# Optimization experiments

Hardware: AMD Instinct MI355X
Metric: run time of the kernel (lower is better)

The kernel has to match this reference:

```python
import jax, jax.numpy as jnp
import numpy as np

NC, NU, K, C, P, O = 20, 16, 128, 2048, 5, 256

def setup_inputs() -> dict:
    key = jax.random.key(0)
    ks = jax.random.split(key, 6)
    s = 0.02  # keep activations well-scaled
    return {
        "topk_feats": jax.random.normal(ks[0], (NC, NU, K, C), jnp.float32),
        "prototypes": jax.random.normal(ks[1], (NC, P, C), jnp.float32),
        "w_inner1": jax.random.normal(ks[2], (O, C), jnp.float32) * s,
        "w_inner_trans": jax.random.normal(ks[3], (C, C), jnp.float32) * s,
        "w_inter1": jax.random.normal(ks[4], (O, C), jnp.float32) * s,
        "w_inter2": jax.random.normal(ks[5], (O, C), jnp.float32) * s,
    }

def reference(topk_feats, prototypes, w_inner1, w_inner_trans, w_inter1, w_inter2):
    scale = 1.0 / jnp.sqrt(jnp.asarray(O, topk_feats.dtype))
    # --- inner (per-group) self-attention, vmapped over (class, unlabel) ---
    # fe: [nc, nu, k, o]
    fe = jnp.einsum("nukc,oc->nuko", topk_feats, w_inner1)
    att = jax.nn.softmax(jnp.einsum("nuko,nulo->nukl", fe, fe) * scale, axis=-1)
    agg = jnp.einsum("nukl,nulc->nukc", att, topk_feats)  # atte @ feat
    feats = topk_feats + jax.nn.relu(jnp.einsum("nukc,dc->nukd", agg, w_inner_trans))
    # --- inter (prototype -> all feats) cross-attention per class ---
    fa = feats.reshape(NC, NU * K, C)  # cat over unlabel dim
    fae = jnp.einsum("nmc,oc->nmo", fa, w_inter1)
    pe = jnp.einsum("npc,oc->npo", prototypes, w_inter2)
    att2 = jax.nn.softmax(jnp.einsum("npo,nmo->npm", pe, fae) * scale, axis=-1)
    un_protos = jnp.einsum("npm,nmc->npc", att2, fa)  # [nc, p, c]
    return un_protos
```

## Files before the change

kernel.cpp:

```cpp
#include <hip/hip_runtime.h>

typedef __attribute__((ext_vector_type(4))) float f32x4;
typedef __attribute__((ext_vector_type(8))) short short8;

#define DEVI static __device__ __forceinline__

DEVI unsigned short f2bf(float f) {
  unsigned int u = __float_as_uint(f);
  u += 0x7FFFu + ((u >> 16) & 1u);
  return (unsigned short)(u >> 16);
}
DEVI float bf2f(unsigned short s) { return __uint_as_float(((unsigned int)s) << 16); }
DEVI unsigned int pack2(float lo, float hi) {
  return ((unsigned int)f2bf(hi) << 16) | (unsigned int)f2bf(lo);
}

#define GL2LDS(gp, lp)                                                        \
  __builtin_amdgcn_global_load_lds(                                           \
      (const __attribute__((address_space(1))) void*)(const void*)(gp),       \
      (__attribute__((address_space(3))) void*)(void*)(lp), 16, 0, 0)

__global__ __launch_bounds__(256) void k_cvt_bf16(const float* __restrict__ src,
                                                  unsigned short* __restrict__ dst, int n4) {
  int i = blockIdx.x * 256 + threadIdx.x;
  if (i < n4) {
    float4 v = ((const float4*)src)[i];
    uint2 o; o.x = pack2(v.x, v.y); o.y = pack2(v.z, v.w);
    ((uint2*)dst)[i] = o;
  }
}

template <bool RES>
__global__ __launch_bounds__(256) void k_gemm_bt(const unsigned short* __restrict__ A,
                                                 const unsigned short* __restrict__ B,
                                                 unsigned short* __restrict__ C,
                                                 const float* __restrict__ resid, int N) {
  constexpr int K = 2048;
  __shared__ unsigned short lA[2][128 * 64];
  __shared__ unsigned short lB[2][128 * 64];
  const int tid = threadIdx.x;
  const int lane = tid & 63;
  const int wave = tid >> 6;
  const int wr = wave >> 1, wc = wave & 1;
  const int nx = gridDim.x;
  const int lin = blockIdx.y * nx + blockIdx.x;
  const int cpx = (nx * gridDim.y) >> 3;
  const int swz = (lin & 7) * cpx + (lin >> 3);
  const long mBase = (long)(swz / nx) * 128;
  const long nBase = (long)(swz % nx) * 128;

  f32x4 acc[4][4] = {};

  auto stage = [&](int buf, int k0) {
#pragma unroll
    for (int it = 0; it < 4; it++) {
      int idx = it * 256 + tid;
      int row = idx >> 3, kc = idx & 7;
      int skc = kc ^ (row & 7);
      int lbase = (it * 256 + (tid & ~63)) * 8;
      GL2LDS(A + (mBase + row) * (long)K + k0 + skc * 8, &lA[buf][lbase]);
      GL2LDS(B + (nBase + row) * (long)K + k0 + skc * 8, &lB[buf][lbase]);
    }
  };

  stage(0, 0);
  for (int t = 0; t < 32; t++) {
    const int cur = t & 1;
    if (t < 31) {
      stage(cur ^ 1, (t + 1) * 64);
      asm volatile("s_waitcnt vmcnt(8)" ::: "memory");
    } else {
      asm volatile("s_waitcnt vmcnt(0)" ::: "memory");
    }
    __builtin_amdgcn_s_barrier();
    __builtin_amdgcn_sched_barrier(0);
    const unsigned short* bA = &lA[cur][0];
    const unsigned short* bB = &lB[cur][0];
#pragma unroll
    for (int kb = 0; kb < 2; kb++) {
      short8 af[4], bfr[4];
#pragma unroll
      for (int mt = 0; mt < 4; mt++) {
        int row = wr * 64 + mt * 16 + (lane & 15);
        int slot = (kb * 4 + (lane >> 4)) ^ (row & 7);
        af[mt] = *(const short8*)&bA[row * 64 + slot * 8];
      }
#pragma unroll
      for (int nt = 0; nt < 4; nt++) {
        int row = wc * 64 + nt * 16 + (lane & 15);
        int slot = (kb * 4 + (lane >> 4)) ^ (row & 7);
        bfr[nt] = *(const short8*)&bB[row * 64 + slot * 8];
      }
#pragma unroll
      for (int mt = 0; mt < 4; mt++)
#pragma unroll
        for (int nt = 0; nt < 4; nt++)
          acc[mt][nt] = __builtin_amdgcn_mfma_f32_16x16x32_bf16(af[mt], bfr[nt], acc[mt][nt], 0, 0, 0);
    }
    __builtin_amdgcn_sched_barrier(0);
    __builtin_amdgcn_s_barrier();
  }
#pragma unroll
  for (int mt = 0; mt < 4; mt++) {
#pragma unroll
    for (int nt = 0; nt < 4; nt++) {
#pragma unroll
      for (int j = 0; j < 4; j++) {
        long row = mBase + wr * 64 + mt * 16 + (lane >> 4) * 4 + j;
        long col = nBase + wc * 64 + nt * 16 + (lane & 15);
        float v = acc[mt][nt][j];
        if constexpr (RES) v = resid[row * (long)N + col] + fmaxf(v, 0.0f);
        C[row * (long)N + col] = f2bf(v);
      }
    }
  }
}

template <bool RES>
__global__ __launch_bounds__(512, 2) void k_gemm256(const unsigned short* __restrict__ A,
                                                    const unsigned short* __restrict__ B,
                                                    unsigned short* __restrict__ C,
                                                    const float* __restrict__ resid, int N) {
  constexpr int K = 2048;
  __shared__ unsigned short lA[2][256 * 64];
  __shared__ unsigned short lB[2][256 * 64];
  const int tid = threadIdx.x;
  const int lane = tid & 63;
  const int wave = tid >> 6;
  const int wr = wave >> 2, wc = wave & 3;
  const int lin = blockIdx.y * 8 + blockIdx.x;
  const int swz = (lin & 7) * 160 + (lin >> 3);
  const long mBase = (long)(swz >> 3) * 256;
  const long nBase = (long)(swz & 7) * 256;

  f32x4 acc[8][4] = {};

  auto stage = [&](int buf, int k0) {
#pragma unroll
    for (int it = 0; it < 4; it++) {
      int idx = it * 512 + tid;
      int row = idx >> 3, kc = idx & 7;
      int skc = kc ^ (row & 7);
      int lbase = (it * 512 + (tid & ~63)) * 8;
      GL2LDS(A + (mBase + row) * (long)K + k0 + skc * 8, &lA[buf][lbase]);
      GL2LDS(B + (nBase + row) * (long)K + k0 + skc * 8, &lB[buf][lbase]);
    }
  };

  stage(0, 0);
  for (int t = 0; t < 32; t++) {
    const int cur = t & 1;
    if (t < 31) {
      stage(cur ^ 1, (t + 1) * 64);
      asm volatile("s_waitcnt vmcnt(8)" ::: "memory");
    } else {
      asm volatile("s_waitcnt vmcnt(0)" ::: "memory");
    }
    __builtin_amdgcn_s_barrier();
    __builtin_amdgcn_sched_barrier(0);
    const unsigned short* bA = &lA[cur][0];
    const unsigned short* bB = &lB[cur][0];
#pragma unroll
    for (int kb = 0; kb < 2; kb++) {
      short8 af[8], bfr[4];
#pragma unroll
      for (int mt = 0; mt < 8; mt++) {
        int row = wr * 128 + mt * 16 + (lane & 15);
        int slot = (kb * 4 + (lane >> 4)) ^ (row & 7);
        af[mt] = *(const short8*)&bA[row * 64 + slot * 8];
      }
#pragma unroll
      for (int nt = 0; nt < 4; nt++) {
        int row = wc * 64 + nt * 16 + (lane & 15);
        int slot = (kb * 4 + (lane >> 4)) ^ (row & 7);
        bfr[nt] = *(const short8*)&bB[row * 64 + slot * 8];
      }
#pragma unroll
      for (int mt = 0; mt < 8; mt++)
#pragma unroll
        for (int nt = 0; nt < 4; nt++)
          acc[mt][nt] = __builtin_amdgcn_mfma_f32_16x16x32_bf16(af[mt], bfr[nt], acc[mt][nt], 0, 0, 0);
    }
    __builtin_amdgcn_sched_barrier(0);
    __builtin_amdgcn_s_barrier();
  }
#pragma unroll
  for (int mt = 0; mt < 8; mt++) {
#pragma unroll
    for (int nt = 0; nt < 4; nt++) {
#pragma unroll
      for (int j = 0; j < 4; j++) {
        long row = mBase + wr * 128 + mt * 16 + (lane >> 4) * 4 + j;
        long col = nBase + wc * 64 + nt * 16 + (lane & 15);
        float v = acc[mt][nt][j];
        if constexpr (RES) v = resid[row * (long)N + col] + fmaxf(v, 0.0f);
        C[row * (long)N + col] = f2bf(v);
      }
    }
  }
}

__global__ __launch_bounds__(256) void k_attn_inner(const unsigned short* __restrict__ fe,
                                                    const unsigned short* __restrict__ topkb,
                                                    unsigned short* __restrict__ agg) {
  __shared__ unsigned short attb[128 * 136];
  __shared__ unsigned short featT[64 * 128];
  __shared__ float redmax[2 * 128];
  __shared__ float redsum[2 * 128];
  const int tid = threadIdx.x;
  const int lane = tid & 63;
  const int wave = tid >> 6;
  const int wr = wave >> 1, wc = wave & 1;
  const int g = blockIdx.x;
  const unsigned short* feG = fe + (long)g * 128 * 256;

  f32x4 s[4][4] = {};
#pragma unroll
  for (int kb = 0; kb < 8; kb++) {
    short8 af[4], bfr[4];
#pragma unroll
    for (int mt = 0; mt < 4; mt++) {
      int row = wr * 64 + mt * 16 + (lane & 15);
      af[mt] = *(const short8*)(feG + row * 256 + kb * 32 + (lane >> 4) * 8);
    }
#pragma unroll
    for (int nt = 0; nt < 4; nt++) {
      int row = wc * 64 + nt * 16 + (lane & 15);
      bfr[nt] = *(const short8*)(feG + row * 256 + kb * 32 + (lane >> 4) * 8);
    }
#pragma unroll
    for (int mt = 0; mt < 4; mt++)
#pragma unroll
      for (int nt = 0; nt < 4; nt++)
        s[mt][nt] = __builtin_amdgcn_mfma_f32_16x16x32_bf16(af[mt], bfr[nt], s[mt][nt], 0, 0, 0);
  }

  const float cexp = 0.0625f * 1.44269504088896f;
#pragma unroll
  for (int mt = 0; mt < 4; mt++) {
#pragma unroll
    for (int j = 0; j < 4; j++) {
      float m = fmaxf(fmaxf(s[mt][0][j], s[mt][1][j]), fmaxf(s[mt][2][j], s[mt][3][j]));
#pragma unroll
      for (int d = 1; d < 16; d <<= 1) m = fmaxf(m, __shfl_xor(m, d, 64));
      int r = wr * 64 + mt * 16 + (lane >> 4) * 4 + j;
      if ((lane & 15) == 0) redmax[wc * 128 + r] = m;
    }
  }
  __syncthreads();
#pragma unroll
  for (int mt = 0; mt < 4; mt++) {
#pragma unroll
    for (int j = 0; j < 4; j++) {
      int r = wr * 64 + mt * 16 + (lane >> 4) * 4 + j;
      float M = fmaxf(redmax[r], redmax[128 + r]);
      float sm = 0.f;
#pragma unroll
      for (int nt = 0; nt < 4; nt++) {
        float p = exp2f((s[mt][nt][j] - M) * cexp);
        s[mt][nt][j] = p;
        sm += p;
      }
#pragma unroll
      for (int d = 1; d < 16; d <<= 1) sm += __shfl_xor(sm, d, 64);
      if ((lane & 15) == 0) redsum[wc * 128 + r] = sm;
    }
  }
  __syncthreads();
#pragma unroll
  for (int mt = 0; mt < 4; mt++) {
#pragma unroll
    for (int j = 0; j < 4; j++) {
      int r = wr * 64 + mt * 16 + (lane >> 4) * 4 + j;
      float inv = 1.0f / (redsum[r] + redsum[128 + r]);
#pragma unroll
      for (int nt = 0; nt < 4; nt++) {
        int c = wc * 64 + nt * 16 + (lane & 15);
        attb[r * 136 + c] = f2bf(s[mt][nt][j] * inv);
      }
    }
  }

  for (int ch = 0; ch < 32; ch++) {
    __syncthreads();
#pragma unroll
    for (int i = 0; i < 4; i++) {
      int seg = i * 256 + tid;
      int l = seg >> 3, kc = seg & 7;
      const unsigned short* gp = topkb + ((long)g * 128 + l) * 2048 + ch * 64 + kc * 8;
      uint4 w = *(const uint4*)gp;
      unsigned short v[8];
      v[0] = (unsigned short)(w.x & 0xffff); v[1] = (unsigned short)(w.x >> 16);
      v[2] = (unsigned short)(w.y & 0xffff); v[3] = (unsigned short)(w.y >> 16);
      v[4] = (unsigned short)(w.z & 0xffff); v[5] = (unsigned short)(w.z >> 16);
      v[6] = (unsigned short)(w.w & 0xffff); v[7] = (unsigned short)(w.w >> 16);
      int lx = l ^ (kc << 3);
#pragma unroll
      for (int j = 0; j < 8; j++) featT[(kc * 8 + j) * 128 + lx] = v[j];
    }
    __syncthreads();
    f32x4 c[2][4] = {};
#pragma unroll
    for (int kb = 0; kb < 4; kb++) {
      short8 af2[2], bf2v[4];
#pragma unroll
      for (int mt = 0; mt < 2; mt++) {
        int r = wave * 32 + mt * 16 + (lane & 15);
        af2[mt] = *(const short8*)&attb[r * 136 + kb * 32 + (lane >> 4) * 8];
      }
#pragma unroll
      for (int nt = 0; nt < 4; nt++) {
        int cc = nt * 16 + (lane & 15);
        int l0 = (kb * 32 + (lane >> 4) * 8) ^ (((cc >> 3) & 7) << 3);
        bf2v[nt] = *(const short8*)&featT[cc * 128 + l0];
      }
#pragma unroll
      for (int mt = 0; mt < 2; mt++)
#pragma unroll
        for (int nt = 0; nt < 4; nt++)
          c[mt][nt] = __builtin_amdgcn_mfma_f32_16x16x32_bf16(af2[mt], bf2v[nt], c[mt][nt], 0, 0, 0);
    }
#pragma unroll
    for (int mt = 0; mt < 2; mt++)
#pragma unroll
      for (int nt = 0; nt < 4; nt++)
#pragma unroll
        for (int j = 0; j < 4; j++) {
          long row = (long)g * 128 + wave * 32 + mt * 16 + (lane >> 4) * 4 + j;
          int col = ch * 64 + nt * 16 + (lane & 15);
          agg[row * 2048 + col] = f2bf(c[mt][nt][j]);
        }
  }
}

__global__ __launch_bounds__(256) void k_pe(const float* __restrict__ protos,
                                            const float* __restrict__ wi2,
                                            float* __restrict__ pe) {
  int n = blockIdx.x, oc = blockIdx.y, tid = threadIdx.x;
  if (tid < 160) {
    int p = tid >> 5, o = oc * 32 + (tid & 31);
    const float* pr = protos + ((long)n * 5 + p) * 2048;
    const float* wr = wi2 + (long)o * 2048;
    float acc = 0.f;
    for (int cidx = 0; cidx < 2048; cidx += 4) {
      float4 a = *(const float4*)(pr + cidx);
      float4 b = *(const float4*)(wr + cidx);
      acc += a.x * b.x + a.y * b.y + a.z * b.z + a.w * b.w;
    }
    pe[((long)n * 5 + p) * 256 + o] = acc;
  }
}

__global__ __launch_bounds__(256) void k_q(const float* __restrict__ pe,
                                           const float* __restrict__ wi1,
                                           float* __restrict__ q) {
  __shared__ float pel[1280];
  int n = blockIdx.x, cb = blockIdx.y, tid = threadIdx.x;
  for (int i = tid; i < 1280; i += 256) pel[i] = pe[(long)n * 1280 + i];
  __syncthreads();
  int c = cb * 256 + tid;
  float a[5] = {0.f, 0.f, 0.f, 0.f, 0.f};
  for (int o = 0; o < 256; o++) {
    float w = wi1[(long)o * 2048 + c];
#pragma unroll
    for (int p = 0; p < 5; p++) a[p] += pel[p * 256 + o] * w;
  }
#pragma unroll
  for (int p = 0; p < 5; p++) q[((long)n * 5 + p) * 2048 + c] = a[p];
}

__global__ __launch_bounds__(256) void k_lg(const float* __restrict__ q,
                                            const unsigned short* __restrict__ feats,
                                            float* __restrict__ lgp) {
  __shared__ float ql[5 * 1024];
  int n = blockIdx.x, mc = blockIdx.y, cb = blockIdx.z, tid = threadIdx.x;
  const float4* qs = (const float4*)(q + (long)n * 5 * 2048);
  for (int i = tid; i < 1280; i += 256) {
    int p = i >> 8, r = i & 255;
    ((float4*)ql)[i] = qs[p * 512 + cb * 256 + r];
  }
  __syncthreads();
  int m = mc * 256 + tid;
  const unsigned short* fr = feats + ((long)n * 2048 + m) * 2048 + cb * 1024;
  float a[5] = {0.f, 0.f, 0.f, 0.f, 0.f};
  for (int c = 0; c < 1024; c += 8) {
    uint4 w = *(const uint4*)(fr + c);
    float f[8];
    f[0] = bf2f((unsigned short)(w.x & 0xffff)); f[1] = bf2f((unsigned short)(w.x >> 16));
    f[2] = bf2f((unsigned short)(w.y & 0xffff)); f[3] = bf2f((unsigned short)(w.y >> 16));
    f[4] = bf2f((unsigned short)(w.z & 0xffff)); f[5] = bf2f((unsigned short)(w.z >> 16));
    f[6] = bf2f((unsigned short)(w.w & 0xffff)); f[7] = bf2f((unsigned short)(w.w >> 16));
#pragma unroll
    for (int j = 0; j < 8; j++) {
      float fv = f[j];
#pragma unroll
      for (int p = 0; p < 5; p++) a[p] += fv * ql[p * 1024 + c + j];
    }
  }
#pragma unroll
  for (int p = 0; p < 5; p++)
    lgp[((long)cb * 100 + n * 5 + p) * 2048 + m] = a[p] * 0.0625f;
}

__global__ __launch_bounds__(256) void k_sm(const float* __restrict__ lgp,
                                            float* __restrict__ att2) {
  __shared__ float red[4], red2[4];
  int b = blockIdx.x, tid = threadIdx.x;
  const float* s0 = lgp + (long)b * 2048;
  const float* s1 = lgp + (long)100 * 2048 + (long)b * 2048;
  float v[8];
  float mx = -1e30f;
#pragma unroll
  for (int i = 0; i < 8; i++) {
    v[i] = s0[i * 256 + tid] + s1[i * 256 + tid];
    mx = fmaxf(mx, v[i]);
  }
#pragma unroll
  for (int d = 1; d < 64; d <<= 1) mx = fmaxf(mx, __shfl_xor(mx, d, 64));
  if ((tid & 63) == 0) red[tid >> 6] = mx;
  __syncthreads();
  mx = fmaxf(fmaxf(red[0], red[1]), fmaxf(red[2], red[3]));
  float sm = 0.f;
#pragma unroll
  for (int i = 0; i < 8; i++) { v[i] = exp2f((v[i] - mx) * 1.44269504088896f); sm += v[i]; }
#pragma unroll
  for (int d = 1; d < 64; d <<= 1) sm += __shfl_xor(sm, d, 64);
  if ((tid & 63) == 0) red2[tid >> 6] = sm;
  __syncthreads();
  float inv = 1.0f / (red2[0] + red2[1] + red2[2] + red2[3]);
  float* dst = att2 + (long)b * 2048;
#pragma unroll
  for (int i = 0; i < 8; i++) dst[i * 256 + tid] = v[i] * inv;
}

__global__ __launch_bounds__(256) void k_out_part(const float* __restrict__ att2,
                                                  const unsigned short* __restrict__ feats,
                                                  float* __restrict__ partial) {
  __shared__ float a2[5 * 512];
  int n = blockIdx.x, cb = blockIdx.y, ms = blockIdx.z;
  int tid = threadIdx.x;
  const float* src = att2 + (long)n * 5 * 2048 + ms * 512;
  for (int i = tid; i < 640; i += 256) {
    int p = i >> 7, qq = i & 127;
    ((float4*)a2)[i] = *(const float4*)(src + p * 2048 + qq * 4);
  }
  __syncthreads();
  int c0 = cb * 512 + tid * 2;
  const unsigned short* fp = feats + ((long)n * 2048 + ms * 512) * 2048 + c0;
  float acc[5][2] = {};
  for (int m = 0; m < 512; m++) {
    unsigned int w = *(const unsigned int*)(fp + (long)m * 2048);
    float f0 = bf2f((unsigned short)(w & 0xffff));
    float f1 = bf2f((unsigned short)(w >> 16));
#pragma unroll
    for (int p = 0; p < 5; p++) {
      float a = a2[p * 512 + m];
      acc[p][0] += a * f0;
      acc[p][1] += a * f1;
    }
  }
  float* pp = partial + ((long)ms * 100 + (long)n * 5) * 2048;
#pragma unroll
  for (int p = 0; p < 5; p++) {
    float2 o; o.x = acc[p][0]; o.y = acc[p][1];
    *(float2*)(pp + p * 2048 + c0) = o;
  }
}

__global__ __launch_bounds__(256) void k_out_red(const float* __restrict__ partial,
                                                 float* __restrict__ outp) {
  int i = blockIdx.x * 256 + threadIdx.x;
  const f32x4* P = (const f32x4*)partial;
  f32x4 s = P[i] + P[51200 + i] + P[2 * 51200 + i] + P[3 * 51200 + i];
  ((f32x4*)outp)[i] = s;
}

extern "C" void kernel_launch(void* const* d_in, const int* in_sizes, int n_in,
                              void* d_out, int out_size, void* d_ws, size_t ws_size,
                              hipStream_t stream) {
  const float* topk = (const float*)d_in[0];
  const float* protos = (const float*)d_in[1];
  const float* w1 = (const float*)d_in[2];
  const float* wt = (const float*)d_in[3];
  const float* wi1 = (const float*)d_in[4];
  const float* wi2 = (const float*)d_in[5];
  float* outp = (float*)d_out;

  char* ws = (char*)d_ws;
  size_t off = 0;
  auto alloc = [&](size_t bytes) -> void* {
    void* p = ws + off;
    off += (bytes + 255) & ~(size_t)255;
    return p;
  };
  unsigned short* w1b = (unsigned short*)alloc((size_t)256 * 2048 * 2);
  unsigned short* wtb = (unsigned short*)alloc((size_t)2048 * 2048 * 2);
  unsigned short* topkb = (unsigned short*)alloc((size_t)40960 * 2048 * 2);
  unsigned short* fe = (unsigned short*)alloc((size_t)40960 * 256 * 2);
  unsigned short* agg = (unsigned short*)alloc((size_t)40960 * 2048 * 2);
  float* pe = (float*)alloc((size_t)20 * 5 * 256 * 4);
  float* q = (float*)alloc((size_t)20 * 5 * 2048 * 4);
  float* lgp = (float*)alloc((size_t)2 * 100 * 2048 * 4);
  float* att2 = (float*)alloc((size_t)20 * 5 * 2048 * 4);
  float* partial = (float*)alloc((size_t)4 * 100 * 2048 * 4);
  unsigned short* feats = topkb;

  k_cvt_bf16<<<512, 256, 0, stream>>>(w1, w1b, 131072);
  k_cvt_bf16<<<4096, 256, 0, stream>>>(wt, wtb, 1048576);
  k_cvt_bf16<<<81920, 256, 0, stream>>>(topk, topkb, 20971520);

  k_gemm_bt<false><<<dim3(2, 320), 256, 0, stream>>>(topkb, w1b, fe, nullptr, 256);
  k_attn_inner<<<320, 256, 0, stream>>>(fe, topkb, agg);
  k_gemm256<true><<<dim3(8, 160), 512, 0, stream>>>(agg, wtb, feats, topk, 2048);
  k_pe<<<dim3(20, 8), 256, 0, stream>>>(protos, wi2, pe);
  k_q<<<dim3(20, 8), 256, 0, stream>>>(pe, wi1, q);
  k_lg<<<dim3(20, 8, 2), 256, 0, stream>>>(q, feats, lgp);
  k_sm<<<100, 256, 0, stream>>>(lgp, att2);
  k_out_part<<<dim3(20, 4, 4), 256, 0, stream>>>(att2, feats, partial);
  k_out_red<<<200, 256, 0, stream>>>(partial, outp);
}
```

Before: 982.2 us.

## Restructure big GEMM into 8-phase half-tile pipelined schedule with bf16 residual

Rewrites the 256x256 GEMM main loop so LDS buffers are split into halves and global-to-LDS loads for future k-steps are interleaved with four MFMA quadrants per iteration, using s_setprio and explicit barriers. Occupancy drops to one block per CU. The residual add now reads the bf16 copy of topk instead of fp32, which halves the residual traffic but rounds the residual to bf16, and it aliases the output buffer (each element is read, then written by the same thread). The aim is to hide load latency and shorten LDS waits, in exchange for more barriers and fewer resident blocks.

After: 898.8 us. -8.5%, faster.

```diff
diff --git a/kernel.cpp b/kernel.cpp
--- a/kernel.cpp
+++ b/kernel.cpp
@@ -19,6 +19,13 @@
   __builtin_amdgcn_global_load_lds(                                           \
       (const __attribute__((address_space(1))) void*)(const void*)(gp),       \
       (__attribute__((address_space(3))) void*)(void*)(lp), 16, 0, 0)
+
+#define BARRIER __builtin_amdgcn_s_barrier()
+#define LGKM0                                                                 \
+  do {                                                                        \
+    asm volatile("s_waitcnt lgkmcnt(0)" ::: "memory");                        \
+    __builtin_amdgcn_sched_barrier(0);                                        \
+  } while (0)
 
 __global__ __launch_bounds__(256) void k_cvt_bf16(const float* __restrict__ src,
                                                   unsigned short* __restrict__ dst, int n4) {
@@ -117,13 +124,14 @@
 }
 
 template <bool RES>
-__global__ __launch_bounds__(512, 2) void k_gemm256(const unsigned short* __restrict__ A,
-                                                    const unsigned short* __restrict__ B,
-                                                    unsigned short* __restrict__ C,
-                                                    const float* __restrict__ resid, int N) {
+__global__ __launch_bounds__(512, 1) void k_gemm256_8p(const unsigned short* __restrict__ A,
+                                                       const unsigned short* __restrict__ B,
+                                                       unsigned short* __restrict__ C,
+                                                       const unsigned short* __restrict__ residb,
+                                                       int N) {
   constexpr int K = 2048;
-  __shared__ unsigned short lA[2][256 * 64];
-  __shared__ unsigned short lB[2][256 * 64];
+  __shared__ unsigned short lA[2][2][128 * 64];
+  __shared__ unsigned short lB[2][2][128 * 64];
   const int tid = threadIdx.x;
   const int lane = tid & 63;
   const int wave = tid >> 6;
@@ -134,56 +142,100 @@
   const long nBase = (long)(swz & 7) * 256;
 
   f32x4 acc[8][4] = {};
-
-  auto stage = [&](int buf, int k0) {
-#pragma unroll
-    for (int it = 0; it < 4; it++) {
-      int idx = it * 512 + tid;
-      int row = idx >> 3, kc = idx & 7;
-      int skc = kc ^ (row & 7);
-      int lbase = (it * 512 + (tid & ~63)) * 8;
-      GL2LDS(A + (mBase + row) * (long)K + k0 + skc * 8, &lA[buf][lbase]);
-      GL2LDS(B + (nBase + row) * (long)K + k0 + skc * 8, &lB[buf][lbase]);
-    }
-  };
-
-  stage(0, 0);
+  short8 af[4][2];
+  short8 bfr[4][2];
+
+  auto stageA = [&](int buf, int half, int t) {
+    const unsigned short* base = A + (mBase + half * 128) * (long)K + (long)t * 64;
+    unsigned short* lds = &lA[buf][half][0];
+#pragma unroll
+    for (int it = 0; it < 2; it++) {
+      int r = it * 64 + (tid >> 3);
+      int kc = tid & 7;
+      int skc = kc ^ (r & 7);
+      GL2LDS(base + (long)r * K + skc * 8, lds + (it * 512 + (tid & ~63)) * 8);
+    }
+  };
+  auto stageB = [&](int buf, int half, int t) {
+    const unsigned short* base = B + (nBase + half * 128) * (long)K + (long)t * 64;
+    unsigned short* lds = &lB[buf][half][0];
+#pragma unroll
+    for (int it = 0; it < 2; it++) {
+      int r = it * 64 + (tid >> 3);
+      int kc = tid & 7;
+      int skc = kc ^ (r & 7);
+      GL2LDS(base + (long)r * K + skc * 8, lds + (it * 512 + (tid & ~63)) * 8);
+    }
+  };
+  auto readA = [&](int buf, int mhalf) {
+#pragma unroll
+    for (int mt = 0; mt < 4; mt++)
+#pragma unroll
+      for (int kb = 0; kb < 2; kb++) {
+        int r = mhalf * 64 + mt * 16 + (lane & 15);
+        int slot = (kb * 4 + (lane >> 4)) ^ (r & 7);
+        af[mt][kb] = *(const short8*)&lA[buf][wr][r * 64 + slot * 8];
+      }
+  };
+  auto readB = [&](int buf, int nh) {
+#pragma unroll
+    for (int ntl = 0; ntl < 2; ntl++)
+#pragma unroll
+      for (int kb = 0; kb < 2; kb++) {
+        int nt = nh * 2 + ntl;
+        int col = wc * 64 + nt * 16 + (lane & 15);
+        int half = col >> 7, r = col & 127;
+        int slot = (kb * 4 + (lane >> 4)) ^ (r & 7);
+        bfr[nt][kb] = *(const short8*)&lB[buf][half][r * 64 + slot * 8];
+      }
+  };
+  auto mfmaQ = [&](int mhalf, int nh) {
+    __builtin_amdgcn_s_setprio(1);
+#pragma unroll
+    for (int kb = 0; kb < 2; kb++)
+#pragma unroll
+      for (int mt = 0; mt < 4; mt++)
+#pragma unroll
+        for (int ntl = 0; ntl < 2; ntl++) {
+          int nt = nh * 2 + ntl;
+          acc[mhalf * 4 + mt][nt] = __builtin_amdgcn_mfma_f32_16x16x32_bf16(
+              af[mt][kb], bfr[nt][kb], acc[mhalf * 4 + mt][nt], 0, 0, 0);
+        }
+    __builtin_amdgcn_s_setprio(0);
+  };
+
+  stageA(0, 0, 0); stageA(0, 1, 0); stageB(0, 0, 0); stageB(0, 1, 0);
+  stageA(1, 0, 1); stageA(1, 1, 1); stageB(1, 0, 1); stageB(1, 1, 1);
+  asm volatile("s_waitcnt vmcnt(8)" ::: "memory");
+  BARRIER;
+
   for (int t = 0; t < 32; t++) {
     const int cur = t & 1;
-    if (t < 31) {
-      stage(cur ^ 1, (t + 1) * 64);
-      asm volatile("s_waitcnt vmcnt(8)" ::: "memory");
-    } else {
+    readA(cur, 0);
+    readB(cur, 0);
+    if (t >= 1 && t <= 30) stageA(cur ^ 1, 1, t + 1);
+    BARRIER; LGKM0;
+    mfmaQ(0, 0);
+    BARRIER;
+    readB(cur, 1);
+    BARRIER; LGKM0;
+    mfmaQ(0, 1);
+    BARRIER;
+    readA(cur, 1);
+    if (t <= 29) stageB(cur, 0, t + 2);
+    BARRIER; LGKM0;
+    mfmaQ(1, 0);
+    BARRIER;
+    if (t <= 29) { stageB(cur, 1, t + 2); stageA(cur, 0, t + 2); }
+    mfmaQ(1, 1);
+    if (t <= 29) {
+      asm volatile("s_waitcnt vmcnt(6)" ::: "memory");
+    } else if (t == 30) {
       asm volatile("s_waitcnt vmcnt(0)" ::: "memory");
     }
-    __builtin_amdgcn_s_barrier();
-    __builtin_amdgcn_sched_barrier(0);
-    const unsigned short* bA = &lA[cur][0];
-    const unsigned short* bB = &lB[cur][0];
-#pragma unroll
-    for (int kb = 0; kb < 2; kb++) {
-      short8 af[8], bfr[4];
-#pragma unroll
-      for (int mt = 0; mt < 8; mt++) {
-        int row = wr * 128 + mt * 16 + (lane & 15);
-        int slot = (kb * 4 + (lane >> 4)) ^ (row & 7);
-        af[mt] = *(const short8*)&bA[row * 64 + slot * 8];
-      }
-#pragma unroll
-      for (int nt = 0; nt < 4; nt++) {
-        int row = wc * 64 + nt * 16 + (lane & 15);
-        int slot = (kb * 4 + (lane >> 4)) ^ (row & 7);
-        bfr[nt] = *(const short8*)&bB[row * 64 + slot * 8];
-      }
-#pragma unroll
-      for (int mt = 0; mt < 8; mt++)
-#pragma unroll
-        for (int nt = 0; nt < 4; nt++)
-          acc[mt][nt] = __builtin_amdgcn_mfma_f32_16x16x32_bf16(af[mt], bfr[nt], acc[mt][nt], 0, 0, 0);
-    }
-    __builtin_amdgcn_sched_barrier(0);
-    __builtin_amdgcn_s_barrier();
-  }
+    BARRIER;
+  }
+
 #pragma unroll
   for (int mt = 0; mt < 8; mt++) {
 #pragma unroll
@@ -193,7 +245,7 @@
         long row = mBase + wr * 128 + mt * 16 + (lane >> 4) * 4 + j;
         long col = nBase + wc * 64 + nt * 16 + (lane & 15);
         float v = acc[mt][nt][j];
-        if constexpr (RES) v = resid[row * (long)N + col] + fmaxf(v, 0.0f);
+        if constexpr (RES) v = bf2f(residb[row * (long)N + col]) + fmaxf(v, 0.0f);
         C[row * (long)N + col] = f2bf(v);
       }
     }
@@ -511,7 +563,7 @@
 
   k_gemm_bt<false><<<dim3(2, 320), 256, 0, stream>>>(topkb, w1b, fe, nullptr, 256);
   k_attn_inner<<<320, 256, 0, stream>>>(fe, topkb, agg);
-  k_gemm256<true><<<dim3(8, 160), 512, 0, stream>>>(agg, wtb, feats, topk, 2048);
+  k_gemm256_8p<true><<<dim3(8, 160), 512, 0, stream>>>(agg, wtb, feats, topkb, 2048);
   k_pe<<<dim3(20, 8), 256, 0, stream>>>(protos, wi2, pe);
   k_q<<<dim3(20, 8), 256, 0, stream>>>(pe, wi1, q);
   k_lg<<<dim3(20, 8, 2), 256, 0, stream>>>(q, feats, lgp);
```
